# Performance work log

Hardware: AMD Instinct MI355X
Metric: run time of the kernel (lower is better)

The kernel has to match this reference:

```python
import jax, jax.numpy as jnp
import numpy as np

B_SZ, L, D, N = 4, 2048, 768, 16


def setup_inputs() -> dict:
    key = jax.random.key(0)
    ks = jax.random.split(key, 8)
    x = jax.random.normal(ks[0], (B_SZ, L, D), dtype=jnp.float32)
    # A_log initialized as log(arange(1..N)) repeated over d, as in the module
    A_log = jnp.log(jnp.broadcast_to(jnp.arange(1, N + 1, dtype=jnp.float32), (D, N)))
    # s_b_c: Linear(D, 2N)
    W_bc = jax.random.normal(ks[1], (2 * N, D), dtype=jnp.float32) / jnp.sqrt(D)
    b_bc = jnp.zeros((2 * N,), dtype=jnp.float32)
    # s_1: Linear(D, 1)
    W_1 = jax.random.normal(ks[2], (1, D), dtype=jnp.float32) / jnp.sqrt(D)
    b_1 = jnp.zeros((1,), dtype=jnp.float32)
    # s_delta: Linear(1, D)
    W_d = jax.random.normal(ks[3], (D, 1), dtype=jnp.float32)
    b_d = jnp.zeros((D,), dtype=jnp.float32)
    return {"x": x, "A_log": A_log, "W_bc": W_bc, "b_bc": b_bc,
            "W_1": W_1, "b_1": b_1, "W_d": W_d, "b_d": b_d}


def reference(x, A_log, W_bc, b_bc, W_1, b_1, W_d, b_d):
    b, l, d = x.shape
    n = A_log.shape[1]
    A = -jnp.exp(A_log)                                   # (d, n)
    BandC = x @ W_bc.T + b_bc                             # (b, l, 2n)
    Bm, Cm = BandC[..., :n], BandC[..., n:]               # (b, l, n) each
    # delta = softplus(s_delta(s_1(x)))  -> (b, l, d)
    s1 = x @ W_1.T + b_1                                  # (b, l, 1)
    delta = jax.nn.softplus(s1 @ W_d.T + b_d)             # (b, l, d)
    deltaA = jnp.exp(jnp.einsum('bld,dn->bldn', delta, A))        # (b, l, d, n)
    deltaB_u = jnp.einsum('bld,bln,bld->bldn', delta, Bm, x)      # (b, l, d, n)

    # sequential selective-scan over time with lax.scan
    dA_t = jnp.moveaxis(deltaA, 1, 0)      # (l, b, d, n)
    dBu_t = jnp.moveaxis(deltaB_u, 1, 0)   # (l, b, d, n)
    C_t = jnp.moveaxis(Cm, 1, 0)           # (l, b, n)

    def step(h, inp):
        dA_i, dBu_i, c_i = inp
        h = dA_i * h + dBu_i               # (b, d, n)
        y = jnp.einsum('bdn,bn->bd', h, c_i)
        return h, y

    h0 = jnp.zeros((b, d, n), dtype=x.dtype)
    _, ys = jax.lax.scan(step, h0, (dA_t, dBu_t, C_t))
    return jnp.moveaxis(ys, 0, 1)          # (b, l, d)
```

## Files before the change

kernel.cpp:

```cpp
#include <hip/hip_runtime.h>

#define L_SEQ 2048
#define D_DIM 768
#define N_ST 16
#define NB 4
#define NJ 33

__device__ __forceinline__ float fast_exp2(float x) {
#if __has_builtin(__builtin_amdgcn_exp2f)
  return __builtin_amdgcn_exp2f(x);
#else
  return __expf(x * 0.69314718055994531f);
#endif
}

__device__ __forceinline__ float softplus_f(float v) {
  float e = __expf(v);
  float l = __logf(1.0f + e);
  return (v > 15.0f) ? v : l;
}

__global__ __launch_bounds__(256) void k_proj(
    const float* __restrict__ x, const float* __restrict__ W_bc,
    const float* __restrict__ b_bc, const float* __restrict__ W_1,
    const float* __restrict__ b_1, float* __restrict__ BC33) {
  const int lane = threadIdx.x & 63;
  const int wave = threadIdx.x >> 6;
  const int bl0 = blockIdx.x * 16 + wave * 4;
  const float* x0 = x + (size_t)bl0 * D_DIM;

  float xv[4][12];
#pragma unroll
  for (int t = 0; t < 4; ++t)
#pragma unroll
    for (int k = 0; k < 12; ++k)
      xv[t][k] = x0[t * D_DIM + k * 64 + lane];

  float r0 = 0.f, r1 = 0.f, r2 = 0.f, r3 = 0.f;
  for (int j = 0; j < NJ; ++j) {
    const float* wr = (j < 32) ? (W_bc + j * D_DIM) : W_1;
    float a0 = 0.f, a1 = 0.f, a2 = 0.f, a3 = 0.f;
#pragma unroll
    for (int k = 0; k < 12; ++k) {
      float wv = wr[k * 64 + lane];
      a0 = fmaf(xv[0][k], wv, a0);
      a1 = fmaf(xv[1][k], wv, a1);
      a2 = fmaf(xv[2][k], wv, a2);
      a3 = fmaf(xv[3][k], wv, a3);
    }
#pragma unroll
    for (int off = 32; off >= 1; off >>= 1) {
      a0 += __shfl_xor(a0, off);
      a1 += __shfl_xor(a1, off);
      a2 += __shfl_xor(a2, off);
      a3 += __shfl_xor(a3, off);
    }
    float bias = (j < 32) ? b_bc[j] : b_1[0];
    if (lane == j) { r0 = a0 + bias; r1 = a1 + bias; r2 = a2 + bias; r3 = a3 + bias; }
  }
  if (lane < NJ) {
    BC33[(size_t)(bl0 + 0) * NJ + lane] = r0;
    BC33[(size_t)(bl0 + 1) * NJ + lane] = r1;
    BC33[(size_t)(bl0 + 2) * NJ + lane] = r2;
    BC33[(size_t)(bl0 + 3) * NJ + lane] = r3;
  }
}

template <int LC>
__global__ __launch_bounds__(256) void k_scan1(
    const float* __restrict__ x, const float* __restrict__ A_log,
    const float* __restrict__ W_d, const float* __restrict__ b_d,
    const float* __restrict__ BC33, float* __restrict__ P,
    float* __restrict__ H, int NC) {
  const int cb = blockIdx.x % 3;
  const int c  = (blockIdx.x / 3) % NC;
  const int b  = blockIdx.x / (3 * NC);
  const int d  = cb * 256 + threadIdx.x;

  const float wd = W_d[d], bd = b_d[d];
  float Aln[N_ST];
#pragma unroll
  for (int n = 0; n < N_ST; ++n)
    Aln[n] = -__expf(A_log[d * N_ST + n]) * 1.44269504088896f;

  float h[N_ST];
#pragma unroll
  for (int n = 0; n < N_ST; ++n) h[n] = 0.0f;
  float dsum = 0.0f;

  const int l0 = c * LC;
  const float* bc = BC33 + (size_t)(b * L_SEQ + l0) * NJ;
  const float* xp = x + (size_t)(b * L_SEQ + l0) * D_DIM + d;

#pragma unroll 8
  for (int l = 0; l < LC; ++l) {
    float s1 = bc[l * NJ + 32];
    float delta = softplus_f(fmaf(s1, wd, bd));
    float xv = xp[(size_t)l * D_DIM];
    float f = delta * xv;
    dsum += delta;
#pragma unroll
    for (int n = 0; n < N_ST; ++n) {
      float dA = fast_exp2(delta * Aln[n]);
      h[n] = fmaf(dA, h[n], f * bc[l * NJ + n]);
    }
  }

  size_t base = ((size_t)(b * NC + c) * D_DIM + d) * N_ST;
  float4* P4 = (float4*)(P + base);
  float4* H4 = (float4*)(H + base);
#pragma unroll
  for (int q = 0; q < 4; ++q) {
    P4[q] = make_float4(fast_exp2(Aln[4*q+0] * dsum), fast_exp2(Aln[4*q+1] * dsum),
                        fast_exp2(Aln[4*q+2] * dsum), fast_exp2(Aln[4*q+3] * dsum));
    H4[q] = make_float4(h[4*q], h[4*q+1], h[4*q+2], h[4*q+3]);
  }
}

__global__ __launch_bounds__(256) void k_combine(
    const float* __restrict__ P, float* __restrict__ H, int NC) {
  const int b  = blockIdx.x / 48;
  const int tl = (blockIdx.x % 48) * 256 + threadIdx.x;
  float h = 0.0f;
#pragma unroll 4
  for (int c = 0; c < NC; ++c) {
    size_t idx = (size_t)(b * NC + c) * (D_DIM * N_ST) + tl;
    float hold = H[idx];
    float p = P[idx];
    H[idx] = h;
    h = fmaf(p, h, hold);
  }
}

template <int LC>
__global__ __launch_bounds__(256) void k_scan2(
    const float* __restrict__ x, const float* __restrict__ A_log,
    const float* __restrict__ W_d, const float* __restrict__ b_d,
    const float* __restrict__ BC33, const float* __restrict__ HIN,
    float* __restrict__ out, int NC) {
  const int cb = blockIdx.x % 3;
  const int c  = (blockIdx.x / 3) % NC;
  const int b  = blockIdx.x / (3 * NC);
  const int d  = cb * 256 + threadIdx.x;

  const float wd = W_d[d], bd = b_d[d];
  float Aln[N_ST];
#pragma unroll
  for (int n = 0; n < N_ST; ++n)
    Aln[n] = -__expf(A_log[d * N_ST + n]) * 1.44269504088896f;

  float h[N_ST];
  size_t base = ((size_t)(b * NC + c) * D_DIM + d) * N_ST;
  const float4* HIN4 = (const float4*)(HIN + base);
#pragma unroll
  for (int q = 0; q < 4; ++q) {
    float4 v = HIN4[q];
    h[4*q] = v.x; h[4*q+1] = v.y; h[4*q+2] = v.z; h[4*q+3] = v.w;
  }

  const int l0 = c * LC;
  const float* bc = BC33 + (size_t)(b * L_SEQ + l0) * NJ;
  const float* xp = x + (size_t)(b * L_SEQ + l0) * D_DIM + d;
  float* op = out + (size_t)(b * L_SEQ + l0) * D_DIM + d;

#pragma unroll 8
  for (int l = 0; l < LC; ++l) {
    float s1 = bc[l * NJ + 32];
    float delta = softplus_f(fmaf(s1, wd, bd));
    float xv = xp[(size_t)l * D_DIM];
    float f = delta * xv;
    float y = 0.0f;
#pragma unroll
    for (int n = 0; n < N_ST; ++n) {
      float dA = fast_exp2(delta * Aln[n]);
      h[n] = fmaf(dA, h[n], f * bc[l * NJ + n]);
      y = fmaf(h[n], bc[l * NJ + 16 + n], y);
    }
    op[(size_t)l * D_DIM] = y;
  }
}

extern "C" void kernel_launch(void* const* d_in, const int* in_sizes, int n_in,
                              void* d_out, int out_size, void* d_ws, size_t ws_size,
                              hipStream_t stream) {
  const float* x     = (const float*)d_in[0];
  const float* A_log = (const float*)d_in[1];
  const float* W_bc  = (const float*)d_in[2];
  const float* b_bc  = (const float*)d_in[3];
  const float* W_1   = (const float*)d_in[4];
  const float* b_1   = (const float*)d_in[5];
  const float* W_d   = (const float*)d_in[6];
  const float* b_d   = (const float*)d_in[7];
  float* out = (float*)d_out;
  float* ws  = (float*)d_ws;

  int NC = 8;
  const int cands[4] = {128, 64, 32, 16};
  for (int i = 0; i < 4; ++i) {
    size_t need = (270336ull + 2ull * 49152ull * cands[i]) * 4ull;
    if (ws_size >= need) { NC = cands[i]; break; }
  }

  float* BC33 = ws;
  float* P    = ws + 270336;
  float* H    = P + (size_t)49152 * NC;

  k_proj<<<512, 256, 0, stream>>>(x, W_bc, b_bc, W_1, b_1, BC33);

  const int gs = 3 * NB * NC;
  switch (NC) {
    case 128:
      k_scan1<16><<<gs, 256, 0, stream>>>(x, A_log, W_d, b_d, BC33, P, H, NC);
      k_combine<<<192, 256, 0, stream>>>(P, H, NC);
      k_scan2<16><<<gs, 256, 0, stream>>>(x, A_log, W_d, b_d, BC33, H, out, NC);
      break;
    case 64:
      k_scan1<32><<<gs, 256, 0, stream>>>(x, A_log, W_d, b_d, BC33, P, H, NC);
      k_combine<<<192, 256, 0, stream>>>(P, H, NC);
      k_scan2<32><<<gs, 256, 0, stream>>>(x, A_log, W_d, b_d, BC33, H, out, NC);
      break;
    case 32:
      k_scan1<64><<<gs, 256, 0, stream>>>(x, A_log, W_d, b_d, BC33, P, H, NC);
      k_combine<<<192, 256, 0, stream>>>(P, H, NC);
      k_scan2<64><<<gs, 256, 0, stream>>>(x, A_log, W_d, b_d, BC33, H, out, NC);
      break;
    case 16:
      k_scan1<128><<<gs, 256, 0, stream>>>(x, A_log, W_d, b_d, BC33, P, H, NC);
      k_combine<<<192, 256, 0, stream>>>(P, H, NC);
      k_scan2<128><<<gs, 256, 0, stream>>>(x, A_log, W_d, b_d, BC33, H, out, NC);
      break;
    default:
      k_scan1<256><<<gs, 256, 0, stream>>>(x, A_log, W_d, b_d, BC33, P, H, NC);
      k_combine<<<192, 256, 0, stream>>>(P, H, NC);
      k_scan2<256><<<gs, 256, 0, stream>>>(x, A_log, W_d, b_d, BC33, H, out, NC);
      break;
  }
}
```

Measured before the change: 187.1 us.

## Tile projection GEMM through LDS with split-K reduce; compute chunk decay in combine

Replaces the per-wave shuffle-reduction projection kernel with an LDS-tiled GEMM that splits the 768-wide reduction into 8 segments, followed by a separate reduce kernel that sums partials and adds biases. Separately, scan1 now writes only the per-chunk delta sum instead of a full 16-wide decay tensor P, and combine recomputes the decay with exp2 and prefetches the next chunk. The aim is to cut the projection's shuffle overhead and the P write and read traffic. The cost is an extra kernel launch and a partial-sum buffer of about 8x the projection size.

Result: faster. 179.4 us (-4.1%).

```diff
diff --git a/kernel.cpp b/kernel.cpp
--- a/kernel.cpp
+++ b/kernel.cpp
@@ -5,6 +5,16 @@
 #define N_ST 16
 #define NB 4
 #define NJ 33
+#define NROWS (NB * L_SEQ)
+#define PROJ_ELEMS (NROWS * NJ)
+
+#define DSPLIT 8
+#define DSEG (D_DIM / DSPLIT)
+#define DK 32
+#define NCHUNK (DSEG / DK)
+#define RB 128
+#define XST 132
+#define WST 64
 
 __device__ __forceinline__ float fast_exp2(float x) {
 #if __has_builtin(__builtin_amdgcn_exp2f)
@@ -20,57 +30,106 @@
   return (v > 15.0f) ? v : l;
 }
 
-__global__ __launch_bounds__(256) void k_proj(
+__global__ __launch_bounds__(256) void k_proj_gemm(
     const float* __restrict__ x, const float* __restrict__ W_bc,
-    const float* __restrict__ b_bc, const float* __restrict__ W_1,
+    const float* __restrict__ W_1, float* __restrict__ PBC) {
+  __shared__ float xs_t[DK * XST];
+  __shared__ float ws_t[DK * WST];
+
+  const int ds  = blockIdx.x % DSPLIT;
+  const int rb0 = (blockIdx.x / DSPLIT) * RB;
+  const int dbase = ds * DSEG;
+  const int tid = threadIdx.x;
+
+  const int rg = tid & 31;
+  const int jg = tid >> 5;
+
+  float acc[4][5];
+#pragma unroll
+  for (int i = 0; i < 4; ++i)
+#pragma unroll
+    for (int k = 0; k < 5; ++k) acc[i][k] = 0.0f;
+
+  const int lrow = tid >> 1;
+  const int lhalf = (tid & 1) * 16;
+  const float* xg_row = x + (size_t)(rb0 + lrow) * D_DIM + dbase + lhalf;
+
+  for (int ch = 0; ch < NCHUNK; ++ch) {
+    const int dc = dbase + ch * DK;
+    float4 xv[4];
+#pragma unroll
+    for (int q = 0; q < 4; ++q)
+      xv[q] = *(const float4*)(xg_row + ch * DK + q * 4);
+    float wv[8];
+    int widx[8];
+#pragma unroll
+    for (int u = 0; u < 8; ++u) {
+      int idx = tid + u * 256;
+      int dk = idx >> 6, slot = idx & 63;
+      int wjg = slot >> 3, wk = slot & 7;
+      int j = wjg + 8 * wk;
+      float v = 0.0f;
+      if (wk < 5) {
+        if (j < 32)       v = W_bc[(size_t)j * D_DIM + dc + dk];
+        else if (j == 32) v = W_1[dc + dk];
+      }
+      wv[u] = v; widx[u] = dk * WST + slot;
+    }
+    __syncthreads();
+#pragma unroll
+    for (int q = 0; q < 4; ++q) {
+      xs_t[(lhalf + q * 4 + 0) * XST + lrow] = xv[q].x;
+      xs_t[(lhalf + q * 4 + 1) * XST + lrow] = xv[q].y;
+      xs_t[(lhalf + q * 4 + 2) * XST + lrow] = xv[q].z;
+      xs_t[(lhalf + q * 4 + 3) * XST + lrow] = xv[q].w;
+    }
+#pragma unroll
+    for (int u = 0; u < 8; ++u) ws_t[widx[u]] = wv[u];
+    __syncthreads();
+#pragma unroll 8
+    for (int dk = 0; dk < DK; ++dk) {
+      float4 xr = *(const float4*)&xs_t[dk * XST + rg * 4];
+      float4 wr = *(const float4*)&ws_t[dk * WST + jg * 8];
+      float w4  = ws_t[dk * WST + jg * 8 + 4];
+      float xa[4] = {xr.x, xr.y, xr.z, xr.w};
+      float wa[5] = {wr.x, wr.y, wr.z, wr.w, w4};
+#pragma unroll
+      for (int i = 0; i < 4; ++i)
+#pragma unroll
+        for (int k = 0; k < 5; ++k)
+          acc[i][k] = fmaf(xa[i], wa[k], acc[i][k]);
+    }
+  }
+
+  float* pb = PBC + (size_t)ds * PROJ_ELEMS;
+#pragma unroll
+  for (int i = 0; i < 4; ++i) {
+    int row = rb0 + rg * 4 + i;
+#pragma unroll
+    for (int k = 0; k < 5; ++k) {
+      int j = jg + 8 * k;
+      if (k < 4 || jg == 0) pb[(size_t)row * NJ + j] = acc[i][k];
+    }
+  }
+}
+
+__global__ __launch_bounds__(256) void k_proj_reduce(
+    const float* __restrict__ PBC, const float* __restrict__ b_bc,
     const float* __restrict__ b_1, float* __restrict__ BC33) {
-  const int lane = threadIdx.x & 63;
-  const int wave = threadIdx.x >> 6;
-  const int bl0 = blockIdx.x * 16 + wave * 4;
-  const float* x0 = x + (size_t)bl0 * D_DIM;
-
-  float xv[4][12];
-#pragma unroll
-  for (int t = 0; t < 4; ++t)
-#pragma unroll
-    for (int k = 0; k < 12; ++k)
-      xv[t][k] = x0[t * D_DIM + k * 64 + lane];
-
-  float r0 = 0.f, r1 = 0.f, r2 = 0.f, r3 = 0.f;
-  for (int j = 0; j < NJ; ++j) {
-    const float* wr = (j < 32) ? (W_bc + j * D_DIM) : W_1;
-    float a0 = 0.f, a1 = 0.f, a2 = 0.f, a3 = 0.f;
-#pragma unroll
-    for (int k = 0; k < 12; ++k) {
-      float wv = wr[k * 64 + lane];
-      a0 = fmaf(xv[0][k], wv, a0);
-      a1 = fmaf(xv[1][k], wv, a1);
-      a2 = fmaf(xv[2][k], wv, a2);
-      a3 = fmaf(xv[3][k], wv, a3);
-    }
-#pragma unroll
-    for (int off = 32; off >= 1; off >>= 1) {
-      a0 += __shfl_xor(a0, off);
-      a1 += __shfl_xor(a1, off);
-      a2 += __shfl_xor(a2, off);
-      a3 += __shfl_xor(a3, off);
-    }
-    float bias = (j < 32) ? b_bc[j] : b_1[0];
-    if (lane == j) { r0 = a0 + bias; r1 = a1 + bias; r2 = a2 + bias; r3 = a3 + bias; }
-  }
-  if (lane < NJ) {
-    BC33[(size_t)(bl0 + 0) * NJ + lane] = r0;
-    BC33[(size_t)(bl0 + 1) * NJ + lane] = r1;
-    BC33[(size_t)(bl0 + 2) * NJ + lane] = r2;
-    BC33[(size_t)(bl0 + 3) * NJ + lane] = r3;
-  }
+  const int idx = blockIdx.x * 256 + threadIdx.x;
+  const int j = idx % NJ;
+  float s = 0.0f;
+#pragma unroll
+  for (int k = 0; k < DSPLIT; ++k) s += PBC[(size_t)k * PROJ_ELEMS + idx];
+  s += (j < 32) ? b_bc[j] : b_1[0];
+  BC33[idx] = s;
 }
 
 template <int LC>
 __global__ __launch_bounds__(256) void k_scan1(
     const float* __restrict__ x, const float* __restrict__ A_log,
     const float* __restrict__ W_d, const float* __restrict__ b_d,
-    const float* __restrict__ BC33, float* __restrict__ P,
+    const float* __restrict__ BC33, float* __restrict__ DS,
     float* __restrict__ H, int NC) {
   const int cb = blockIdx.x % 3;
   const int c  = (blockIdx.x / 3) % NC;
@@ -106,29 +165,39 @@
     }
   }
 
+  DS[((size_t)b * NC + c) * D_DIM + d] = dsum;
   size_t base = ((size_t)(b * NC + c) * D_DIM + d) * N_ST;
-  float4* P4 = (float4*)(P + base);
   float4* H4 = (float4*)(H + base);
 #pragma unroll
-  for (int q = 0; q < 4; ++q) {
-    P4[q] = make_float4(fast_exp2(Aln[4*q+0] * dsum), fast_exp2(Aln[4*q+1] * dsum),
-                        fast_exp2(Aln[4*q+2] * dsum), fast_exp2(Aln[4*q+3] * dsum));
+  for (int q = 0; q < 4; ++q)
     H4[q] = make_float4(h[4*q], h[4*q+1], h[4*q+2], h[4*q+3]);
-  }
 }
 
 __global__ __launch_bounds__(256) void k_combine(
-    const float* __restrict__ P, float* __restrict__ H, int NC) {
+    const float* __restrict__ A_log, const float* __restrict__ DS,
+    float* __restrict__ H, int NC) {
   const int b  = blockIdx.x / 48;
   const int tl = (blockIdx.x % 48) * 256 + threadIdx.x;
+  const int d = tl >> 4, n = tl & 15;
+  const float Aln = -__expf(A_log[d * N_ST + n]) * 1.44269504088896f;
+
+  const float* dsp = DS + (size_t)b * NC * D_DIM + d;
+  float* Hp = H + (size_t)b * NC * (D_DIM * N_ST) + tl;
+
   float h = 0.0f;
+  float ds_c = dsp[0];
+  float hold = Hp[0];
 #pragma unroll 4
   for (int c = 0; c < NC; ++c) {
-    size_t idx = (size_t)(b * NC + c) * (D_DIM * N_ST) + tl;
-    float hold = H[idx];
-    float p = P[idx];
-    H[idx] = h;
+    float ds_n = 0.0f, hold_n = 0.0f;
+    if (c + 1 < NC) {
+      ds_n   = dsp[(size_t)(c + 1) * D_DIM];
+      hold_n = Hp[(size_t)(c + 1) * (D_DIM * N_ST)];
+    }
+    float p = fast_exp2(Aln * ds_c);
+    Hp[(size_t)c * (D_DIM * N_ST)] = h;
     h = fmaf(p, h, hold);
+    ds_c = ds_n; hold = hold_n;
   }
 }
 
@@ -197,41 +266,43 @@
   int NC = 8;
   const int cands[4] = {128, 64, 32, 16};
   for (int i = 0; i < 4; ++i) {
-    size_t need = (270336ull + 2ull * 49152ull * cands[i]) * 4ull;
+    size_t need = (9ull * PROJ_ELEMS + (3072ull + 49152ull) * cands[i]) * 4ull;
     if (ws_size >= need) { NC = cands[i]; break; }
   }
 
   float* BC33 = ws;
-  float* P    = ws + 270336;
-  float* H    = P + (size_t)49152 * NC;
-
-  k_proj<<<512, 256, 0, stream>>>(x, W_bc, b_bc, W_1, b_1, BC33);
+  float* PBC  = ws + PROJ_ELEMS;
+  float* DSb  = PBC + (size_t)DSPLIT * PROJ_ELEMS;
+  float* H    = DSb + (size_t)3072 * NC;
+
+  k_proj_gemm<<<(NROWS / RB) * DSPLIT, 256, 0, stream>>>(x, W_bc, W_1, PBC);
+  k_proj_reduce<<<PROJ_ELEMS / 256, 256, 0, stream>>>(PBC, b_bc, b_1, BC33);
 
   const int gs = 3 * NB * NC;
   switch (NC) {
     case 128:
-      k_scan1<16><<<gs, 256, 0, stream>>>(x, A_log, W_d, b_d, BC33, P, H, NC);
-      k_combine<<<192, 256, 0, stream>>>(P, H, NC);
+      k_scan1<16><<<gs, 256, 0, stream>>>(x, A_log, W_d, b_d, BC33, DSb, H, NC);
+      k_combine<<<192, 256, 0, stream>>>(A_log, DSb, H, NC);
       k_scan2<16><<<gs, 256, 0, stream>>>(x, A_log, W_d, b_d, BC33, H, out, NC);
       break;
     case 64:
-      k_scan1<32><<<gs, 256, 0, stream>>>(x, A_log, W_d, b_d, BC33, P, H, NC);
-      k_combine<<<192, 256, 0, stream>>>(P, H, NC);
+      k_scan1<32><<<gs, 256, 0, stream>>>(x, A_log, W_d, b_d, BC33, DSb, H, NC);
+      k_combine<<<192, 256, 0, stream>>>(A_log, DSb, H, NC);
       k_scan2<32><<<gs, 256, 0, stream>>>(x, A_log, W_d, b_d, BC33, H, out, NC);
       break;
     case 32:
-      k_scan1<64><<<gs, 256, 0, stream>>>(x, A_log, W_d, b_d, BC33, P, H, NC);
-      k_combine<<<192, 256, 0, stream>>>(P, H, NC);
+      k_scan1<64><<<gs, 256, 0, stream>>>(x, A_log, W_d, b_d, BC33, DSb, H, NC);
+      k_combine<<<192, 256, 0, stream>>>(A_log, DSb, H, NC);
       k_scan2<64><<<gs, 256, 0, stream>>>(x, A_log, W_d, b_d, BC33, H, out, NC);
       break;
     case 16:
-      k_scan1<128><<<gs, 256, 0, stream>>>(x, A_log, W_d, b_d, BC33, P, H, NC);
-      k_combine<<<192, 256, 0, stream>>>(P, H, NC);
+      k_scan1<128><<<gs, 256, 0, stream>>>(x, A_log, W_d, b_d, BC33, DSb, H, NC);
+      k_combine<<<192, 256, 0, stream>>>(A_log, DSb, H, NC);
       k_scan2<128><<<gs, 256, 0, stream>>>(x, A_log, W_d, b_d, BC33, H, out, NC);
       break;
     default:
-      k_scan1<256><<<gs, 256, 0, stream>>>(x, A_log, W_d, b_d, BC33, P, H, NC);
-      k_combine<<<192, 256, 0, stream>>>(P, H, NC);
+      k_scan1<256><<<gs, 256, 0, stream>>>(x, A_log, W_d, b_d, BC33, DSb, H, NC);
+      k_combine<<<192, 256, 0, stream>>>(A_log, DSb, H, NC);
       k_scan2<256><<<gs, 256, 0, stream>>>(x, A_log, W_d, b_d, BC33, H, out, NC);
       break;
   }
```
